# Kernel optimization log

Measured on AMD Instinct MI355X. Metric: run time of the kernel, lower is better.

Reference implementation:

```python
import jax, jax.numpy as jnp
import numpy as np
import math

IN_C, N_EMBD, HEADS = 256, 512, 8

def setup_inputs() -> dict:
    key = jax.random.key(0)
    ks = jax.random.split(key, 5)
    B, T = 64, 500
    x = jax.random.normal(ks[0], (B, T, IN_C), dtype=jnp.float32)
    # torch Linear: y = x @ W.T + b; store W as [out, in]
    w_attn = jax.random.normal(ks[1], (3 * N_EMBD, IN_C), dtype=jnp.float32) * (1.0 / math.sqrt(IN_C))
    b_attn = jax.random.normal(ks[2], (3 * N_EMBD,), dtype=jnp.float32) * 0.02
    w_proj = jax.random.normal(ks[3], (N_EMBD, N_EMBD), dtype=jnp.float32) * (1.0 / math.sqrt(N_EMBD))
    b_proj = jax.random.normal(ks[4], (N_EMBD,), dtype=jnp.float32) * 0.02
    return {"x": x, "w_attn": w_attn, "b_attn": b_attn, "w_proj": w_proj, "b_proj": b_proj}

def reference(x, w_attn, b_attn, w_proj, b_proj):
    B, T, C = x.shape
    H, D = HEADS, N_EMBD // HEADS
    qkv = jnp.einsum('btc,ec->bte', x, w_attn) + b_attn  # [B,T,3*n_embd]
    q, k, v = jnp.split(qkv, 3, axis=-1)
    # [B,T,n_embd] -> [B,H,T,D]
    q = q.reshape(B, T, H, D).transpose(0, 2, 1, 3)
    k = k.reshape(B, T, H, D).transpose(0, 2, 1, 3)
    v = v.reshape(B, T, H, D).transpose(0, 2, 1, 3)
    att = jnp.einsum('bhtd,bhsd->bhts', q, k) * (1.0 / math.sqrt(D))
    # bias buffer is all-ones: masked_fill(bias==0, -inf) is a no-op
    att = jax.nn.softmax(att, axis=-1)
    y = jnp.einsum('bhts,bhsd->bhtd', att, v)  # [B,H,T,D]
    y = y.transpose(0, 2, 1, 3).reshape(B, T, N_EMBD)
    return jnp.einsum('bte,fe->btf', y, w_proj) + b_proj
```

## Files before the change

kernel.cpp:

```cpp
#include <hip/hip_runtime.h>

typedef _Float16 f16;
typedef _Float16 f16x8 __attribute__((ext_vector_type(8)));
typedef _Float16 f16x2 __attribute__((ext_vector_type(2)));
typedef float    f32x4 __attribute__((ext_vector_type(4)));
typedef float    f32x16 __attribute__((ext_vector_type(16)));
typedef unsigned int u32;

typedef const __attribute__((address_space(1))) void GVOID;
typedef __attribute__((address_space(3))) void LVOID;

static __device__ __forceinline__ f32x4 mfma16(f16x8 a, f16x8 b, f32x4 c) {
  return __builtin_amdgcn_mfma_f32_16x16x32_f16(a, b, c, 0, 0, 0);
}
static __device__ __forceinline__ f32x16 mfma32(f16x8 a, f16x8 b, f32x16 c) {
  return __builtin_amdgcn_mfma_f32_32x32x16_f16(a, b, c, 0, 0, 0);
}
static __device__ __forceinline__ void gl_lds16(const f16* g, f16* l) {
  __builtin_amdgcn_global_load_lds((GVOID*)g, (LVOID*)l, 16, 0, 0);
}
static __device__ __forceinline__ u32 pk(float a, float b) {
  union { f16x2 h; u32 w; } u;
  u.h[0] = (f16)a; u.h[1] = (f16)b;
  return u.w;
}
static __device__ __forceinline__ f16x8 mkfrag(float a0, float a1, float a2, float a3,
                                               float a4, float a5, float a6, float a7) {
  u32 c01 = pk(a0, a1), c23 = pk(a2, a3), c45 = pk(a4, a5), c67 = pk(a6, a7);
  asm("v_permlane32_swap_b32 %0, %1" : "+v"(c01), "+v"(c45));
  asm("v_permlane32_swap_b32 %0, %1" : "+v"(c23), "+v"(c67));
  union { f16x8 h; u32 w[4]; } u;
  u.w[0] = c01; u.w[1] = c23; u.w[2] = c45; u.w[3] = c67;
  return u.h;
}

__global__ __launch_bounds__(256)
void cvt_kernel(const float* __restrict__ s, f16* __restrict__ d, int n) {
  int i = (blockIdx.x * 256 + threadIdx.x) * 8;
  if (i >= n) return;
  float4 v0 = *(const float4*)(s + i);
  float4 v1 = *(const float4*)(s + i + 4);
  f16x8 h;
  h[0] = (f16)v0.x; h[1] = (f16)v0.y; h[2] = (f16)v0.z; h[3] = (f16)v0.w;
  h[4] = (f16)v1.x; h[5] = (f16)v1.y; h[6] = (f16)v1.z; h[7] = (f16)v1.w;
  *(f16x8*)(d + i) = h;
}

template<int EPI, int KD, int NDIM>
__global__ __launch_bounds__(256)
void gemm16(const f16* __restrict__ A, const f16* __restrict__ B,
            const float* __restrict__ bias, f16* __restrict__ outH,
            float* __restrict__ outF) {
  constexpr int NB = NDIM / 128;
  const int cpx = gridDim.x >> 3;
  const int id = blockIdx.x;
  const int g = (id & 7) * cpx + (id >> 3);
  const int mb = g / NB, nb = g - mb * NB;
  const int m0 = mb * 128, n0 = nb * 128;

  __shared__ __align__(16) f16 As[128 * 64];
  __shared__ __align__(16) f16 Bs[128 * 64];
  const int tid = threadIdx.x, lane = tid & 63, wid = tid >> 6;
  const int wm = (wid >> 1) * 64, wn = (wid & 1) * 64;
  const int fr = lane & 15, fg = lane >> 4;
  const int e7 = fr & 7;

  f32x4 acc[4][4] = {};

  for (int k0 = 0; k0 < KD; k0 += 64) {
    __syncthreads();
#pragma unroll
    for (int i = 0; i < 4; ++i) {
      int c = i * 256 + tid;
      int row = c >> 3;
      int col = 8 * ((c & 7) ^ (row & 7));
      gl_lds16(A + (size_t)(m0 + row) * KD + k0 + col, &As[c * 8]);
      gl_lds16(B + (size_t)(n0 + row) * KD + k0 + col, &Bs[c * 8]);
    }
    __syncthreads();
#pragma unroll
    for (int kk = 0; kk < 2; ++kk) {
      const int sa = 8 * ((4 * kk + fg) ^ e7);
      f16x8 af[4], bf[4];
#pragma unroll
      for (int t = 0; t < 4; ++t) {
        af[t] = *(const f16x8*)&As[(wm + t * 16 + fr) * 64 + sa];
        bf[t] = *(const f16x8*)&Bs[(wn + t * 16 + fr) * 64 + sa];
      }
#pragma unroll
      for (int mt = 0; mt < 4; ++mt)
#pragma unroll
        for (int nt = 0; nt < 4; ++nt)
          acc[mt][nt] = mfma16(af[mt], bf[nt], acc[mt][nt]);
    }
  }

  float bv[4];
#pragma unroll
  for (int nt = 0; nt < 4; ++nt) bv[nt] = bias[n0 + wn + nt * 16 + fr];
#pragma unroll
  for (int mt = 0; mt < 4; ++mt) {
    int mg = m0 + wm + mt * 16 + fg * 4;
#pragma unroll
    for (int r = 0; r < 4; ++r)
#pragma unroll
      for (int nt = 0; nt < 4; ++nt) {
        int ng = n0 + wn + nt * 16 + fr;
        float v = acc[mt][nt][r] + bv[nt];
        if (EPI == 0) outH[(size_t)(mg + r) * NDIM + ng] = (f16)v;
        else          outF[(size_t)(mg + r) * NDIM + ng] = v;
      }
  }
}

__global__ __launch_bounds__(256)
void attn_kern(const f16* __restrict__ qkv, f16* __restrict__ Yg) {
  __shared__ __align__(16) f16 Kl[2][64 * 64];
  __shared__ __align__(16) f16 VT[2][64 * 64];
  const int id = blockIdx.x;
  const int g = (id & 7) * 256 + (id >> 3);
  const int bh = g >> 2, qt = g & 3;
  const int b = bh >> 3, h = bh & 7;
  const int tid = threadIdx.x, lane = tid & 63, w = tid >> 6;
  const int l31 = lane & 31, hi = lane >> 5, e7 = l31 & 7;

  const f16* base  = qkv + (size_t)b * 500 * 1536 + h * 64;
  const f16* Kbase = base + 512;
  const f16* Vbase = base + 1024;

  const int q = qt * 128 + w * 32 + l31;
  const int qc = q < 500 ? q : 499;
  f16x8 qf[4];
  const f16* qp = base + (size_t)qc * 1536 + hi * 8;
#pragma unroll
  for (int ds = 0; ds < 4; ++ds) qf[ds] = *(const f16x8*)(qp + 16 * ds);
  const f16 qs = (f16)(0.125f * 1.44269504f);
#pragma unroll
  for (int ds = 0; ds < 4; ++ds)
#pragma unroll
    for (int j = 0; j < 8; ++j) qf[ds][j] *= qs;

  f32x16 O0 = {}, O1 = {};
  float l = 0.f;

  const int kvp = (lane & 31) * 2, dh = (lane >> 5) * 8, d0 = w * 16;
  f16x8 va, vb;
  const f16x8 VZ = {};

  {
#pragma unroll
    for (int i = 0; i < 2; ++i) {
      int c = tid + 256 * i, row = c >> 3;
      int col = 8 * ((c & 7) ^ (row & 7));
      gl_lds16(Kbase + (size_t)row * 1536 + col, &Kl[0][c * 8]);
    }
    const f16* vp = Vbase + (size_t)kvp * 1536 + d0 + dh;
    va = *(const f16x8*)vp; vb = *(const f16x8*)(vp + 1536);
#pragma unroll
    for (int j = 0; j < 8; ++j) {
      f16x2 p2; p2[0] = va[j]; p2[1] = vb[j];
      *(f16x2*)&VT[0][(d0 + dh + j) * 64 + (kvp ^ (j << 3))] = p2;
    }
    __syncthreads();
  }

#pragma unroll 2
  for (int kt = 0; kt < 8; ++kt) {
    const int cur = kt & 1, nxt = cur ^ 1;
    if (kt < 7) {
      const int kvn = (kt + 1) * 64;
#pragma unroll
      for (int i = 0; i < 2; ++i) {
        int c = tid + 256 * i, row = c >> 3;
        int kv = kvn + row; kv = kv < 500 ? kv : 499;
        int col = 8 * ((c & 7) ^ (row & 7));
        gl_lds16(Kbase + (size_t)kv * 1536 + col, &Kl[nxt][c * 8]);
      }
      int kv = kvn + kvp;
      int kc0 = kv < 500 ? kv : 499, kc1 = kv + 1 < 500 ? kv + 1 : 499;
      const f16* vp0 = Vbase + (size_t)kc0 * 1536 + d0 + dh;
      const f16* vp1 = Vbase + (size_t)kc1 * 1536 + d0 + dh;
      va = *(const f16x8*)vp0; vb = *(const f16x8*)vp1;
      if (kv >= 500) va = VZ;
      if (kv + 1 >= 500) vb = VZ;
    }

    f32x16 s0 = {}, s1 = {};
    __builtin_amdgcn_s_setprio(1);
#pragma unroll
    for (int ds = 0; ds < 4; ++ds) {
      f16x8 k0 = *(const f16x8*)&Kl[cur][l31 * 64 + 8 * ((hi + 2 * ds) ^ e7)];
      f16x8 k1 = *(const f16x8*)&Kl[cur][(32 + l31) * 64 + 8 * ((hi + 2 * ds) ^ e7)];
      s0 = mfma32(k0, qf[ds], s0);
      s1 = mfma32(k1, qf[ds], s1);
    }
    __builtin_amdgcn_s_setprio(0);

    if (kt == 7) {
#pragma unroll
      for (int r = 0; r < 16; ++r) {
        int kvL = (r & 3) + 8 * (r >> 2) + 4 * hi;
        if (480 + kvL >= 500) s1[r] = -1e30f;
      }
    }

    float ps = 0.f;
#pragma unroll
    for (int r = 0; r < 16; ++r) {
      float t = __builtin_amdgcn_exp2f(s0[r] - 8.f);
      s0[r] = t; ps += t;
    }
#pragma unroll
    for (int r = 0; r < 16; ++r) {
      float t = __builtin_amdgcn_exp2f(s1[r] - 8.f);
      s1[r] = t; ps += t;
    }
    ps += __shfl_xor(ps, 32);
    l += ps;

    f16x8 pf0 = mkfrag(s0[0], s0[1], s0[2], s0[3], s0[4], s0[5], s0[6], s0[7]);
    f16x8 pf1 = mkfrag(s0[8], s0[9], s0[10], s0[11], s0[12], s0[13], s0[14], s0[15]);
    f16x8 pf2 = mkfrag(s1[0], s1[1], s1[2], s1[3], s1[4], s1[5], s1[6], s1[7]);
    f16x8 pf3 = mkfrag(s1[8], s1[9], s1[10], s1[11], s1[12], s1[13], s1[14], s1[15]);

    __builtin_amdgcn_s_setprio(1);
#pragma unroll
    for (int ks = 0; ks < 4; ++ks) {
      f16x8 pf = ks == 0 ? pf0 : ks == 1 ? pf1 : ks == 2 ? pf2 : pf3;
      int sw = (16 * ks + 8 * hi) ^ (e7 << 3);
      f16x8 v0 = *(const f16x8*)&VT[cur][l31 * 64 + sw];
      f16x8 v1 = *(const f16x8*)&VT[cur][(32 + l31) * 64 + sw];
      O0 = mfma32(pf, v0, O0);
      O1 = mfma32(pf, v1, O1);
    }
    __builtin_amdgcn_s_setprio(0);

    if (kt < 7) {
#pragma unroll
      for (int j = 0; j < 8; ++j) {
        f16x2 p2; p2[0] = va[j]; p2[1] = vb[j];
        *(f16x2*)&VT[nxt][(d0 + dh + j) * 64 + (kvp ^ (j << 3))] = p2;
      }
    }
    __syncthreads();
  }

  float linv = __builtin_amdgcn_rcpf(l);
#pragma unroll
  for (int r = 0; r < 16; ++r) {
    int rowv = (r & 3) + 8 * (r >> 2) + 4 * hi;
    float li = __shfl(linv, rowv);
    int t = qt * 128 + w * 32 + rowv;
    if (t < 500) {
      size_t rowb = (size_t)(b * 500 + t) * 512 + h * 64;
      Yg[rowb + l31]      = (f16)(O0[r] * li);
      Yg[rowb + 32 + l31] = (f16)(O1[r] * li);
    }
  }
}

extern "C" void kernel_launch(void* const* d_in, const int* in_sizes, int n_in,
                              void* d_out, int out_size, void* d_ws, size_t ws_size,
                              hipStream_t stream) {
  const float* x      = (const float*)d_in[0];
  const float* w_attn = (const float*)d_in[1];
  const float* b_attn = (const float*)d_in[2];
  const float* w_proj = (const float*)d_in[3];
  const float* b_proj = (const float*)d_in[4];
  float* out = (float*)d_out;

  char* wsp = (char*)d_ws;
  f16* Yg   = (f16*)wsp;
  f16* x_h  = (f16*)wsp;
  f16* qkv  = (f16*)(wsp + 32768000);
  f16* wa_h = (f16*)(wsp + 32768000 + 98304000);
  f16* wp_h = (f16*)(wsp + 32768000 + 98304000 + 786432);
  if (ws_size < 132382720) return;

  dim3 blk(256);
  cvt_kernel<<<4000, blk, 0, stream>>>(x, x_h, 8192000);
  cvt_kernel<<<192,  blk, 0, stream>>>(w_attn, wa_h, 393216);
  cvt_kernel<<<128,  blk, 0, stream>>>(w_proj, wp_h, 262144);

  gemm16<0, 256, 1536><<<3000, blk, 0, stream>>>(x_h, wa_h, b_attn, qkv, nullptr);
  attn_kern<<<2048, blk, 0, stream>>>(qkv, Yg);
  gemm16<1, 512, 512><<<1000, blk, 0, stream>>>(Yg, wp_h, b_proj, nullptr, out);
}
```

Before: 162.2 us.

## Use 512-thread attention blocks covering 256 queries to halve K/V tile loads

The attention kernel now runs 8 waves per block, each block covering 256 query rows instead of 128, so each (batch, head) is split into 2 query tiles instead of 4. The K and V tiles staged in LDS are shared by twice as many waves, which halves the global K/V traffic and per-block staging work. Each thread now loads one K chunk and a 4-wide V slice. The trade-off is more waves idling at the larger block's barriers and padded query rows past 500 in the second tile, and fewer, larger blocks to schedule.

Result: faster. 146.9 us (-9.4%).

```diff
diff --git a/kernel.cpp b/kernel.cpp
--- a/kernel.cpp
+++ b/kernel.cpp
@@ -2,6 +2,7 @@
 
 typedef _Float16 f16;
 typedef _Float16 f16x8 __attribute__((ext_vector_type(8)));
+typedef _Float16 f16x4 __attribute__((ext_vector_type(4)));
 typedef _Float16 f16x2 __attribute__((ext_vector_type(2)));
 typedef float    f32x4 __attribute__((ext_vector_type(4)));
 typedef float    f32x16 __attribute__((ext_vector_type(16)));
@@ -22,6 +23,11 @@
 static __device__ __forceinline__ u32 pk(float a, float b) {
   union { f16x2 h; u32 w; } u;
   u.h[0] = (f16)a; u.h[1] = (f16)b;
+  return u.w;
+}
+static __device__ __forceinline__ u32 pkh(f16 a, f16 b) {
+  union { f16x2 h; u32 w; } u;
+  u.h[0] = a; u.h[1] = b;
   return u.w;
 }
 static __device__ __forceinline__ f16x8 mkfrag(float a0, float a1, float a2, float a3,
@@ -113,22 +119,22 @@
   }
 }
 
-__global__ __launch_bounds__(256)
+__global__ __launch_bounds__(512, 4)
 void attn_kern(const f16* __restrict__ qkv, f16* __restrict__ Yg) {
   __shared__ __align__(16) f16 Kl[2][64 * 64];
   __shared__ __align__(16) f16 VT[2][64 * 64];
   const int id = blockIdx.x;
-  const int g = (id & 7) * 256 + (id >> 3);
-  const int bh = g >> 2, qt = g & 3;
+  const int g = (id & 7) * 128 + (id >> 3);
+  const int bh = g >> 1, qt = g & 1;
   const int b = bh >> 3, h = bh & 7;
-  const int tid = threadIdx.x, lane = tid & 63, w = tid >> 6;
-  const int l31 = lane & 31, hi = lane >> 5, e7 = l31 & 7;
+  const int tid = threadIdx.x, w = tid >> 6;
+  const int l31 = tid & 31, hi = (tid & 63) >> 5, e7 = l31 & 7;
 
   const f16* base  = qkv + (size_t)b * 500 * 1536 + h * 64;
   const f16* Kbase = base + 512;
   const f16* Vbase = base + 1024;
 
-  const int q = qt * 128 + w * 32 + l31;
+  const int q = qt * 256 + w * 32 + l31;
   const int qc = q < 500 ? q : 499;
   f16x8 qf[4];
   const f16* qp = base + (size_t)qc * 1536 + hi * 8;
@@ -143,23 +149,19 @@
   f32x16 O0 = {}, O1 = {};
   float l = 0.f;
 
-  const int kvp = (lane & 31) * 2, dh = (lane >> 5) * 8, d0 = w * 16;
-  f16x8 va, vb;
-  const f16x8 VZ = {};
+  const int krow = tid >> 3, kcol = 8 * ((tid & 7) ^ (krow & 7));
+  const int kvp = (tid & 31) * 2, d4 = (tid >> 5) * 4;
+  f16x4 va, vb;
+  const f16x4 VZ4 = {};
 
   {
-#pragma unroll
-    for (int i = 0; i < 2; ++i) {
-      int c = tid + 256 * i, row = c >> 3;
-      int col = 8 * ((c & 7) ^ (row & 7));
-      gl_lds16(Kbase + (size_t)row * 1536 + col, &Kl[0][c * 8]);
-    }
-    const f16* vp = Vbase + (size_t)kvp * 1536 + d0 + dh;
-    va = *(const f16x8*)vp; vb = *(const f16x8*)(vp + 1536);
-#pragma unroll
-    for (int j = 0; j < 8; ++j) {
-      f16x2 p2; p2[0] = va[j]; p2[1] = vb[j];
-      *(f16x2*)&VT[0][(d0 + dh + j) * 64 + (kvp ^ (j << 3))] = p2;
+    gl_lds16(Kbase + (size_t)krow * 1536 + kcol, &Kl[0][tid * 8]);
+    const f16* vp0 = Vbase + (size_t)kvp * 1536 + d4;
+    va = *(const f16x4*)vp0; vb = *(const f16x4*)(vp0 + 1536);
+#pragma unroll
+    for (int dd = 0; dd < 4; ++dd) {
+      int d = d4 + dd;
+      *(u32*)&VT[0][d * 64 + (kvp ^ ((d & 7) << 3))] = pkh(va[dd], vb[dd]);
     }
     __syncthreads();
   }
@@ -169,20 +171,14 @@
     const int cur = kt & 1, nxt = cur ^ 1;
     if (kt < 7) {
       const int kvn = (kt + 1) * 64;
-#pragma unroll
-      for (int i = 0; i < 2; ++i) {
-        int c = tid + 256 * i, row = c >> 3;
-        int kv = kvn + row; kv = kv < 500 ? kv : 499;
-        int col = 8 * ((c & 7) ^ (row & 7));
-        gl_lds16(Kbase + (size_t)kv * 1536 + col, &Kl[nxt][c * 8]);
-      }
+      int kr = kvn + krow; kr = kr < 500 ? kr : 499;
+      gl_lds16(Kbase + (size_t)kr * 1536 + kcol, &Kl[nxt][tid * 8]);
       int kv = kvn + kvp;
       int kc0 = kv < 500 ? kv : 499, kc1 = kv + 1 < 500 ? kv + 1 : 499;
-      const f16* vp0 = Vbase + (size_t)kc0 * 1536 + d0 + dh;
-      const f16* vp1 = Vbase + (size_t)kc1 * 1536 + d0 + dh;
-      va = *(const f16x8*)vp0; vb = *(const f16x8*)vp1;
-      if (kv >= 500) va = VZ;
-      if (kv + 1 >= 500) vb = VZ;
+      va = *(const f16x4*)(Vbase + (size_t)kc0 * 1536 + d4);
+      vb = *(const f16x4*)(Vbase + (size_t)kc1 * 1536 + d4);
+      if (kv >= 500) va = VZ4;
+      if (kv + 1 >= 500) vb = VZ4;
     }
 
     f32x16 s0 = {}, s1 = {};
@@ -237,9 +233,9 @@
 
     if (kt < 7) {
 #pragma unroll
-      for (int j = 0; j < 8; ++j) {
-        f16x2 p2; p2[0] = va[j]; p2[1] = vb[j];
-        *(f16x2*)&VT[nxt][(d0 + dh + j) * 64 + (kvp ^ (j << 3))] = p2;
+      for (int dd = 0; dd < 4; ++dd) {
+        int d = d4 + dd;
+        *(u32*)&VT[nxt][d * 64 + (kvp ^ ((d & 7) << 3))] = pkh(va[dd], vb[dd]);
       }
     }
     __syncthreads();
@@ -250,7 +246,7 @@
   for (int r = 0; r < 16; ++r) {
     int rowv = (r & 3) + 8 * (r >> 2) + 4 * hi;
     float li = __shfl(linv, rowv);
-    int t = qt * 128 + w * 32 + rowv;
+    int t = qt * 256 + w * 32 + rowv;
     if (t < 500) {
       size_t rowb = (size_t)(b * 500 + t) * 512 + h * 64;
       Yg[rowb + l31]      = (f16)(O0[r] * li);
@@ -283,6 +279,6 @@
   cvt_kernel<<<128,  blk, 0, stream>>>(w_proj, wp_h, 262144);
 
   gemm16<0, 256, 1536><<<3000, blk, 0, stream>>>(x_h, wa_h, b_attn, qkv, nullptr);
-  attn_kern<<<2048, blk, 0, stream>>>(qkv, Yg);
+  attn_kern<<<1024, dim3(512), 0, stream>>>(qkv, Yg);
   gemm16<1, 512, 512><<<1000, blk, 0, stream>>>(Yg, wp_h, b_proj, nullptr, out);
 }
```
